# Optimization experiments

Hardware: AMD Instinct MI355X
Metric: run time of the kernel (lower is better)

Reference implementation:

```python
import jax, jax.numpy as jnp
import numpy as np

N, D, K = 65536, 1024, 256

def setup_inputs() -> dict:
    key = jax.random.key(0)
    k1, k2 = jax.random.split(key)
    inputs = jax.random.normal(k1, (N, D), dtype=jnp.float32)
    centroids = jax.random.normal(k2, (K, D), dtype=jnp.float32)
    return {"inputs": inputs, "centroids": centroids}

def reference(inputs, centroids):
    # Squared euclidean distances [K, N] without materializing [K, N, D]:
    # ||c||^2 + ||x||^2 - 2 c @ x^T  (same math as sum(square(x[None]-c[:,None]), -1))
    x_sq = jnp.sum(inputs * inputs, axis=1)            # [N]
    c_sq = jnp.sum(centroids * centroids, axis=1)      # [K]
    cross = jnp.einsum('kd,nd->kn', centroids, inputs) # [K, N]
    distances = c_sq[:, None] + x_sq[None, :] - 2.0 * cross  # [K, N]
    assignments = jnp.argmin(distances, axis=0)        # [N], int
    # calculate_loss: sum_c mean(where(assign==c, distances, 0)) over the full
    # [K,N] grid. Since each n matches exactly one cluster c, the per-cluster
    # masked means sum to the global mean of distances.
    loss = jnp.mean(distances)
    return distances, assignments, loss
```

## Files before the change

kernel.cpp:

```cpp
#include <hip/hip_runtime.h>
#include <cstdint>

#define N_PTS 65536
#define DIM   1024
#define K_CL  256
#define BN    128
#define BK    32
#define NT    (DIM / BK)
#define THREADS 512

typedef __bf16 bf16_t;
typedef bf16_t bf16x8 __attribute__((ext_vector_type(8)));
typedef float  f32x4  __attribute__((ext_vector_type(4)));

union U16x8 { uint4 u4; bf16x8 bf; ushort us[8]; };

__device__ __forceinline__ ushort f2bf_rne(float f) {
    uint32_t u = __float_as_uint(f);
    uint32_t r = (u + 0x7FFFu + ((u >> 16) & 1u)) >> 16;
    return (ushort)r;
}
__device__ __forceinline__ float bf2f(ushort b) {
    return __uint_as_float(((uint32_t)b) << 16);
}

__device__ __forceinline__ void gll16(const void* g, void* l) {
    __builtin_amdgcn_global_load_lds(
        (const __attribute__((address_space(1))) void*)g,
        (__attribute__((address_space(3))) void*)l, 16, 0, 0);
}

#define BAR()   __builtin_amdgcn_s_barrier()
#define SCHB()  __builtin_amdgcn_sched_barrier(0)
#define LGKM0() do { asm volatile("s_waitcnt lgkmcnt(0)" ::: "memory"); \
                     __builtin_amdgcn_sched_barrier(0); } while (0)
#define VMCNT(N) do { asm volatile("s_waitcnt vmcnt(" #N ")" ::: "memory"); \
                      __builtin_amdgcn_sched_barrier(0); } while (0)
#define MFMA(ACC, A, B) (ACC) = __builtin_amdgcn_mfma_f32_16x16x32_bf16((A).bf, (B).bf, (ACC), 0, 0, 0)

__global__ __launch_bounds__(128) void km_prep(const float* __restrict__ cent,
                                               ushort* __restrict__ Ahi,
                                               ushort* __restrict__ Alo,
                                               float* __restrict__ csq) {
    const int r  = blockIdx.x;
    const int j  = threadIdx.x;
    const int kt = j >> 2;
    const int gp = j & 3;
    const int s  = (r >> 1) & 3;
    const int d0 = kt * BK + ((gp ^ s) << 3);

    const float* src = cent + r * DIM + d0;
    float4 a = *(const float4*)src;
    float4 b = *(const float4*)(src + 4);
    float v[8] = {a.x, a.y, a.z, a.w, b.x, b.y, b.z, b.w};

    U16x8 hi, lo;
    float ss = 0.f;
#pragma unroll
    for (int i = 0; i < 8; ++i) {
        float f = v[i];
        ss += f * f;
        ushort h = f2bf_rne(f);
        hi.us[i] = h;
        lo.us[i] = f2bf_rne(f - bf2f(h));
    }
    *(uint4*)(Ahi + kt * (K_CL * BK) + r * BK + gp * 8) = hi.u4;
    *(uint4*)(Alo + kt * (K_CL * BK) + r * BK + gp * 8) = lo.u4;

#pragma unroll
    for (int off = 1; off < 64; off <<= 1) ss += __shfl_xor(ss, off);
    __shared__ float ws2[2];
    if ((j & 63) == 0) ws2[j >> 6] = ss;
    __syncthreads();
    if (j == 0) csq[r] = ws2[0] + ws2[1];
}

__global__ __launch_bounds__(THREADS, 2) void km_main(
    const float* __restrict__ x,
    const ushort* __restrict__ Ahi, const ushort* __restrict__ Alo,
    const float* __restrict__ csq,
    float* __restrict__ out_dist, float* __restrict__ out_assign,
    float* __restrict__ partials) {

    __shared__ __align__(16) ushort sAhi[3][K_CL * BK];
    __shared__ __align__(16) ushort sAlo[3][K_CL * BK];
    __shared__ __align__(16) ushort sBhi[2][BN * BK];
    __shared__ __align__(16) ushort sBlo[2][BN * BK];
    __shared__ __align__(16) float  sCsq[K_CL];
    __shared__ __align__(16) float  sXsq[BN];
    __shared__ float sRedV[4 * BN];
    __shared__ int   sRedI[4 * BN];
    __shared__ float sWsum[8];

    const int tid  = threadIdx.x;
    const int blk  = blockIdx.x;
    const int lane = tid & 63;
    const int w    = tid >> 6;
    const int wr   = w >> 1;
    const int wc   = w & 1;
    const int l15  = lane & 15;
    const int l4   = lane >> 4;

    if (tid < K_CL) sCsq[tid] = csq[tid];

    const int bcol = tid >> 2;
    const int bq   = tid & 3;
    const int bs   = (bcol >> 1) & 3;
    const int bOffW = bcol * BK + ((bq ^ bs) << 3);
    const float* xsrc = x + (size_t)(blk * BN + bcol) * DIM + bq * 8;

    float xs_acc = 0.f;

    auto stageA_hi = [&](int kt, int slot) {
        const char* p = (const char*)Ahi + kt * 16384 + tid * 16;
        char* d = (char*)&sAhi[slot][0] + tid * 16;
        gll16(p,        d);
        gll16(p + 8192, d + 8192);
    };
    auto stageA_lo = [&](int kt, int slot) {
        const char* p = (const char*)Alo + kt * 16384 + tid * 16;
        char* d = (char*)&sAlo[slot][0] + tid * 16;
        gll16(p,        d);
        gll16(p + 8192, d + 8192);
    };
    auto writeB = [&](int buf, float4 u, float4 v) {
        float f[8] = {u.x, u.y, u.z, u.w, v.x, v.y, v.z, v.w};
        U16x8 h, l;
#pragma unroll
        for (int i = 0; i < 8; ++i) {
            float a = f[i];
            xs_acc = fmaf(a, a, xs_acc);
            bf16_t hb = (bf16_t)a;
            h.bf[i] = hb;
            l.bf[i] = (bf16_t)(a - (float)hb);
        }
        *(uint4*)&sBhi[buf][bOffW] = h.u4;
        *(uint4*)&sBlo[buf][bOffW] = l.u4;
    };

    int aOff[4], bOff[4];
#pragma unroll
    for (int f = 0; f < 4; ++f) {
        int row  = wr * 64 + f * 16 + l15;
        aOff[f]  = row * BK + ((l4 ^ ((row >> 1) & 3)) << 3);
        int col  = wc * 64 + f * 16 + l15;
        bOff[f]  = col * BK + ((l4 ^ ((col >> 1) & 3)) << 3);
    }

    float4 p0, p1;
    stageA_hi(0, 0); stageA_lo(0, 0);
    stageA_hi(1, 1); stageA_lo(1, 1);
    p0 = *(const float4*)(xsrc);
    p1 = *(const float4*)(xsrc + 4);
    writeB(0, p0, p1);
    p0 = *(const float4*)(xsrc + BK);
    p1 = *(const float4*)(xsrc + BK + 4);
    __syncthreads();

    f32x4 acc[4][4];
#pragma unroll
    for (int i = 0; i < 4; ++i)
#pragma unroll
        for (int q = 0; q < 4; ++q) acc[i][q] = (f32x4){0.f, 0.f, 0.f, 0.f};

    int sa = 0;
    for (int kt = 0; kt < NT; ++kt) {
        const int  sb  = kt & 1;
        const int  s2  = (sa == 0) ? 2 : sa - 1;
        const bool pf1 = (kt + 1 < NT);
        const bool pf2 = (kt + 2 < NT);

        U16x8 ah[4], al[4], bh[4], bl[4];

#pragma unroll
        for (int f = 0; f < 4; ++f) ah[f].u4 = *(const uint4*)&sAhi[sa][aOff[f]];
        bh[0].u4 = *(const uint4*)&sBhi[sb][bOff[0]];
        bl[0].u4 = *(const uint4*)&sBlo[sb][bOff[0]];
        bh[1].u4 = *(const uint4*)&sBhi[sb][bOff[1]];
        bl[1].u4 = *(const uint4*)&sBlo[sb][bOff[1]];
        if (pf2) stageA_hi(kt + 2, s2);
        SCHB();
        BAR();
        LGKM0();
        __builtin_amdgcn_s_setprio(1);
#pragma unroll
        for (int fi = 0; fi < 4; ++fi) MFMA(acc[fi][0], ah[fi], bh[0]);
#pragma unroll
        for (int fi = 0; fi < 4; ++fi) MFMA(acc[fi][1], ah[fi], bh[1]);
#pragma unroll
        for (int fi = 0; fi < 4; ++fi) MFMA(acc[fi][0], ah[fi], bl[0]);
#pragma unroll
        for (int fi = 0; fi < 4; ++fi) MFMA(acc[fi][1], ah[fi], bl[1]);
        __builtin_amdgcn_s_setprio(0);
        BAR();

        bh[2].u4 = *(const uint4*)&sBhi[sb][bOff[2]];
        bl[2].u4 = *(const uint4*)&sBlo[sb][bOff[2]];
        bh[3].u4 = *(const uint4*)&sBhi[sb][bOff[3]];
        bl[3].u4 = *(const uint4*)&sBlo[sb][bOff[3]];
        if (pf2) stageA_lo(kt + 2, s2);
        SCHB();
        BAR();
        LGKM0();
        __builtin_amdgcn_s_setprio(1);
#pragma unroll
        for (int fi = 0; fi < 4; ++fi) MFMA(acc[fi][2], ah[fi], bh[2]);
#pragma unroll
        for (int fi = 0; fi < 4; ++fi) MFMA(acc[fi][3], ah[fi], bh[3]);
#pragma unroll
        for (int fi = 0; fi < 4; ++fi) MFMA(acc[fi][2], ah[fi], bl[2]);
#pragma unroll
        for (int fi = 0; fi < 4; ++fi) MFMA(acc[fi][3], ah[fi], bl[3]);
        __builtin_amdgcn_s_setprio(0);
        BAR();

#pragma unroll
        for (int f = 0; f < 4; ++f) al[f].u4 = *(const uint4*)&sAlo[sa][aOff[f]];
        if (pf1) writeB(sb ^ 1, p0, p1);
        SCHB();
        if (pf2) {
            const float* p = xsrc + (kt + 2) * BK;
            p0 = *(const float4*)p;
            p1 = *(const float4*)(p + 4);
        }
        SCHB();
        BAR();
        LGKM0();
        __builtin_amdgcn_s_setprio(1);
#pragma unroll
        for (int fj = 0; fj < 4; ++fj)
#pragma unroll
            for (int fi = 0; fi < 4; ++fi) MFMA(acc[fi][fj], al[fi], bh[fj]);
        __builtin_amdgcn_s_setprio(0);
        if (pf2) { VMCNT(6); } else { VMCNT(0); }
        BAR();

        sa = (sa == 2) ? 0 : sa + 1;
    }

    {
        float v = xs_acc;
        v += __shfl_xor(v, 1);
        v += __shfl_xor(v, 2);
        if (bq == 0) sXsq[bcol] = v;
    }
    __syncthreads();

    const int colBase = wc * 64;
    float xs[4];
    f32x4 cs[4];
#pragma unroll
    for (int f = 0; f < 4; ++f) {
        xs[f] = sXsq[colBase + f * 16 + l15];
        cs[f] = *(const f32x4*)&sCsq[wr * 64 + f * 16 + l4 * 4];
    }

    float lsum = 0.f;
    float bestv[4];
    int   bestr[4];
#pragma unroll
    for (int f = 0; f < 4; ++f) { bestv[f] = 3.4e38f; bestr[f] = 0; }

#pragma unroll
    for (int fi = 0; fi < 4; ++fi) {
        const int rowB = wr * 64 + fi * 16 + l4 * 4;
#pragma unroll
        for (int fj = 0; fj < 4; ++fj) {
            const int col = blk * BN + colBase + fj * 16 + l15;
            float* outp = out_dist + (size_t)rowB * N_PTS + col;
#pragma unroll
            for (int j = 0; j < 4; ++j) {
                float d = cs[fi][j] + xs[fj] - 2.0f * acc[fi][fj][j];
                outp[(size_t)j * N_PTS] = d;
                lsum += d;
                int r = rowB + j;
                if (d < bestv[fj]) { bestv[fj] = d; bestr[fj] = r; }
            }
        }
    }

#pragma unroll
    for (int fj = 0; fj < 4; ++fj) {
#pragma unroll
        for (int m = 16; m <= 32; m <<= 1) {
            float ov = __shfl_xor(bestv[fj], m);
            int   orr = __shfl_xor(bestr[fj], m);
            if (ov < bestv[fj] || (ov == bestv[fj] && orr < bestr[fj])) {
                bestv[fj] = ov; bestr[fj] = orr;
            }
        }
        if (lane < 16) {
            sRedV[wr * BN + colBase + fj * 16 + lane] = bestv[fj];
            sRedI[wr * BN + colBase + fj * 16 + lane] = bestr[fj];
        }
    }

#pragma unroll
    for (int off = 1; off < 64; off <<= 1) lsum += __shfl_xor(lsum, off);
    if (lane == 0) sWsum[w] = lsum;
    __syncthreads();

    if (tid < BN) {
        float bv = sRedV[tid];
        int   br = sRedI[tid];
#pragma unroll
        for (int q = 1; q < 4; ++q) {
            float v = sRedV[q * BN + tid];
            int   r = sRedI[q * BN + tid];
            if (v < bv || (v == bv && r < br)) { bv = v; br = r; }
        }
        out_assign[blk * BN + tid] = (float)br;
    }
    if (tid == 0) {
        float t = 0.f;
#pragma unroll
        for (int q = 0; q < 8; ++q) t += sWsum[q];
        partials[blk] = t;
    }
}

__global__ __launch_bounds__(512) void km_fin(const float* __restrict__ partials,
                                              float* __restrict__ out_loss) {
    __shared__ float ws[8];
    const int t = threadIdx.x;
    float v = partials[t];
#pragma unroll
    for (int off = 1; off < 64; off <<= 1) v += __shfl_xor(v, off);
    if ((t & 63) == 0) ws[t >> 6] = v;
    __syncthreads();
    if (t == 0) {
        float s = 0.f;
#pragma unroll
        for (int i = 0; i < 8; ++i) s += ws[i];
        out_loss[0] = s / 16777216.0f;
    }
}

extern "C" void kernel_launch(void* const* d_in, const int* in_sizes, int n_in,
                              void* d_out, int out_size, void* d_ws, size_t ws_size,
                              hipStream_t stream) {
    const float* x    = (const float*)d_in[0];
    const float* cent = (const float*)d_in[1];

    float* out        = (float*)d_out;
    float* out_dist   = out;
    float* out_assign = out + (size_t)K_CL * N_PTS;
    float* out_loss   = out_assign + N_PTS;

    char*   ws       = (char*)d_ws;
    float*  csq      = (float*)ws;
    float*  partials = (float*)(ws + 1024);
    ushort* Ahi      = (ushort*)(ws + 4096);
    ushort* Alo      = (ushort*)(ws + 4096 + 524288);

    km_prep<<<dim3(K_CL), dim3(128), 0, stream>>>(cent, Ahi, Alo, csq);
    km_main<<<dim3(N_PTS / BN), dim3(THREADS), 0, stream>>>(
        x, Ahi, Alo, csq, out_dist, out_assign, partials);
    km_fin<<<dim3(1), dim3(512), 0, stream>>>(partials, out_loss);
}
```

Before: 137.2 us.

## Collapse three-phase main loop into a single-barrier iteration with merged A staging

Result: faster. 130.1 us (-5.2%).

```diff
diff --git a/kernel.cpp b/kernel.cpp
--- a/kernel.cpp
+++ b/kernel.cpp
@@ -34,8 +34,6 @@
 #define SCHB()  __builtin_amdgcn_sched_barrier(0)
 #define LGKM0() do { asm volatile("s_waitcnt lgkmcnt(0)" ::: "memory"); \
                      __builtin_amdgcn_sched_barrier(0); } while (0)
-#define VMCNT(N) do { asm volatile("s_waitcnt vmcnt(" #N ")" ::: "memory"); \
-                      __builtin_amdgcn_sched_barrier(0); } while (0)
 #define MFMA(ACC, A, B) (ACC) = __builtin_amdgcn_mfma_f32_16x16x32_bf16((A).bf, (B).bf, (ACC), 0, 0, 0)
 
 __global__ __launch_bounds__(128) void km_prep(const float* __restrict__ cent,
@@ -111,17 +109,15 @@
 
     float xs_acc = 0.f;
 
-    auto stageA_hi = [&](int kt, int slot) {
-        const char* p = (const char*)Ahi + kt * 16384 + tid * 16;
-        char* d = (char*)&sAhi[slot][0] + tid * 16;
-        gll16(p,        d);
-        gll16(p + 8192, d + 8192);
-    };
-    auto stageA_lo = [&](int kt, int slot) {
-        const char* p = (const char*)Alo + kt * 16384 + tid * 16;
-        char* d = (char*)&sAlo[slot][0] + tid * 16;
-        gll16(p,        d);
-        gll16(p + 8192, d + 8192);
+    auto stageA = [&](int kt, int slot) {
+        const char* ph = (const char*)Ahi + (size_t)kt * 16384 + tid * 16;
+        const char* pl = (const char*)Alo + (size_t)kt * 16384 + tid * 16;
+        char* dh = (char*)&sAhi[slot][0] + tid * 16;
+        char* dl = (char*)&sAlo[slot][0] + tid * 16;
+        gll16(ph,        dh);
+        gll16(ph + 8192, dh + 8192);
+        gll16(pl,        dl);
+        gll16(pl + 8192, dl + 8192);
     };
     auto writeB = [&](int buf, float4 u, float4 v) {
         float f[8] = {u.x, u.y, u.z, u.w, v.x, v.y, v.z, v.w};
@@ -148,8 +144,8 @@
     }
 
     float4 p0, p1;
-    stageA_hi(0, 0); stageA_lo(0, 0);
-    stageA_hi(1, 1); stageA_lo(1, 1);
+    stageA(0, 0);
+    stageA(1, 1);
     p0 = *(const float4*)(xsrc);
     p1 = *(const float4*)(xsrc + 4);
     writeB(0, p0, p1);
@@ -165,74 +161,47 @@
 
     int sa = 0;
     for (int kt = 0; kt < NT; ++kt) {
-        const int  sb  = kt & 1;
+        const int  buf = kt & 1;
         const int  s2  = (sa == 0) ? 2 : sa - 1;
         const bool pf1 = (kt + 1 < NT);
         const bool pf2 = (kt + 2 < NT);
 
-        U16x8 ah[4], al[4], bh[4], bl[4];
-
-#pragma unroll
-        for (int f = 0; f < 4; ++f) ah[f].u4 = *(const uint4*)&sAhi[sa][aOff[f]];
-        bh[0].u4 = *(const uint4*)&sBhi[sb][bOff[0]];
-        bl[0].u4 = *(const uint4*)&sBlo[sb][bOff[0]];
-        bh[1].u4 = *(const uint4*)&sBhi[sb][bOff[1]];
-        bl[1].u4 = *(const uint4*)&sBlo[sb][bOff[1]];
-        if (pf2) stageA_hi(kt + 2, s2);
+        U16x8 ah[4], al[4];
+#pragma unroll
+        for (int f = 0; f < 4; ++f) {
+            ah[f].u4 = *(const uint4*)&sAhi[sa][aOff[f]];
+            al[f].u4 = *(const uint4*)&sAlo[sa][aOff[f]];
+        }
+
+        if (pf2) stageA(kt + 2, s2);
         SCHB();
-        BAR();
-        LGKM0();
-        __builtin_amdgcn_s_setprio(1);
-#pragma unroll
-        for (int fi = 0; fi < 4; ++fi) MFMA(acc[fi][0], ah[fi], bh[0]);
-#pragma unroll
-        for (int fi = 0; fi < 4; ++fi) MFMA(acc[fi][1], ah[fi], bh[1]);
-#pragma unroll
-        for (int fi = 0; fi < 4; ++fi) MFMA(acc[fi][0], ah[fi], bl[0]);
-#pragma unroll
-        for (int fi = 0; fi < 4; ++fi) MFMA(acc[fi][1], ah[fi], bl[1]);
-        __builtin_amdgcn_s_setprio(0);
-        BAR();
-
-        bh[2].u4 = *(const uint4*)&sBhi[sb][bOff[2]];
-        bl[2].u4 = *(const uint4*)&sBlo[sb][bOff[2]];
-        bh[3].u4 = *(const uint4*)&sBhi[sb][bOff[3]];
-        bl[3].u4 = *(const uint4*)&sBlo[sb][bOff[3]];
-        if (pf2) stageA_lo(kt + 2, s2);
+
+        if (pf1) writeB(buf ^ 1, p0, p1);
         SCHB();
-        BAR();
-        LGKM0();
-        __builtin_amdgcn_s_setprio(1);
-#pragma unroll
-        for (int fi = 0; fi < 4; ++fi) MFMA(acc[fi][2], ah[fi], bh[2]);
-#pragma unroll
-        for (int fi = 0; fi < 4; ++fi) MFMA(acc[fi][3], ah[fi], bh[3]);
-#pragma unroll
-        for (int fi = 0; fi < 4; ++fi) MFMA(acc[fi][2], ah[fi], bl[2]);
-#pragma unroll
-        for (int fi = 0; fi < 4; ++fi) MFMA(acc[fi][3], ah[fi], bl[3]);
-        __builtin_amdgcn_s_setprio(0);
-        BAR();
-
-#pragma unroll
-        for (int f = 0; f < 4; ++f) al[f].u4 = *(const uint4*)&sAlo[sa][aOff[f]];
-        if (pf1) writeB(sb ^ 1, p0, p1);
-        SCHB();
+
         if (pf2) {
-            const float* p = xsrc + (kt + 2) * BK;
+            const float* p = xsrc + (size_t)(kt + 2) * BK;
             p0 = *(const float4*)p;
             p1 = *(const float4*)(p + 4);
         }
         SCHB();
-        BAR();
+
+        __builtin_amdgcn_s_setprio(1);
+#pragma unroll
+        for (int fj = 0; fj < 4; ++fj) {
+            U16x8 bh, bl;
+            bh.u4 = *(const uint4*)&sBhi[buf][bOff[fj]];
+            bl.u4 = *(const uint4*)&sBlo[buf][bOff[fj]];
+#pragma unroll
+            for (int fi = 0; fi < 4; ++fi) MFMA(acc[fi][fj], ah[fi], bh);
+#pragma unroll
+            for (int fi = 0; fi < 4; ++fi) MFMA(acc[fi][fj], ah[fi], bl);
+#pragma unroll
+            for (int fi = 0; fi < 4; ++fi) MFMA(acc[fi][fj], al[fi], bh);
+        }
+        __builtin_amdgcn_s_setprio(0);
+
         LGKM0();
-        __builtin_amdgcn_s_setprio(1);
-#pragma unroll
-        for (int fj = 0; fj < 4; ++fj)
-#pragma unroll
-            for (int fi = 0; fi < 4; ++fi) MFMA(acc[fi][fj], al[fi], bh[fj]);
-        __builtin_amdgcn_s_setprio(0);
-        if (pf2) { VMCNT(6); } else { VMCNT(0); }
         BAR();
 
         sa = (sa == 2) ? 0 : sa + 1;
```
